# Optimization experiments

Measured on AMD Instinct MI355X. Metric: run time of the kernel, lower is better.

The kernel has to match this reference:

```python
import jax, jax.numpy as jnp
import numpy as np

K = 3       # kernel_size
STRIDE = 1
PAD = 1


def conv2d(x, w, b):
    y = jax.lax.conv_general_dilated(
        x, w, window_strides=(STRIDE, STRIDE), padding=[(PAD, PAD), (PAD, PAD)],
        dimension_numbers=('NCHW', 'OIHW', 'NCHW'))
    return y + b[None, :, None, None]


def setup_inputs() -> dict:
    key = jax.random.key(0)
    ks = jax.random.split(key, 4)
    B, Cin, Cout, H, W = 8, 64, 64, 64, 64
    kk = K * K
    x = jax.random.normal(ks[0], (B, Cin, H, W), jnp.float32)
    # offset / modulator convs (zero-init in the original; use small random weights
    # so offsets are nontrivial but realistic sub-pixel scale)
    w_off = jax.random.normal(ks[1], (2 * kk, Cin, K, K), jnp.float32) * 0.01
    b_off = jnp.zeros((2 * kk,), jnp.float32)
    w_mod = jax.random.normal(ks[2], (kk, Cin, K, K), jnp.float32) * 0.01
    b_mod = jnp.zeros((kk,), jnp.float32)
    # main deformable conv weight, Kaiming-ish scale
    w = jax.random.normal(ks[3], (Cout, Cin, K, K), jnp.float32) * (1.0 / np.sqrt(Cin * kk))
    b = jnp.zeros((Cout,), jnp.float32)
    return {"x": x, "w_off": w_off, "b_off": b_off,
            "w_mod": w_mod, "b_mod": b_mod, "w": w, "b": b}


def deform_conv2d(x, offset, mask, w, b):
    # torchvision deform_conv2d semantics, deformable_groups=1, groups=1.
    B, C, H, W = x.shape
    kk = K * K
    Ho = (H + 2 * PAD - K) // STRIDE + 1
    Wo = (W + 2 * PAD - K) // STRIDE + 1
    # offset channels are interleaved (dy, dx) pairs per kernel tap
    off = offset.reshape(B, kk, 2, Ho, Wo)
    kh, kw = jnp.meshgrid(jnp.arange(K), jnp.arange(K), indexing='ij')
    kh = kh.reshape(kk).astype(x.dtype)
    kw = kw.reshape(kk).astype(x.dtype)
    base_y = (jnp.arange(Ho) * STRIDE - PAD).astype(x.dtype)
    base_x = (jnp.arange(Wo) * STRIDE - PAD).astype(x.dtype)
    # sampling coordinates in input space: [B, kk, Ho, Wo]
    ys = base_y[None, None, :, None] + kh[None, :, None, None] + off[:, :, 0]
    xs = base_x[None, None, None, :] + kw[None, :, None, None] + off[:, :, 1]
    y0 = jnp.floor(ys)
    x0 = jnp.floor(xs)

    def gather(yi, xi):
        yc = jnp.clip(yi, 0, H - 1).astype(jnp.int32)
        xc = jnp.clip(xi, 0, W - 1).astype(jnp.int32)
        # per-batch fancy gather: [C, H, W] indexed by [kk, Ho, Wo] -> [C, kk, Ho, Wo]
        return jax.vmap(lambda img, yb, xb: img[:, yb, xb])(x, yc, xc)

    acc = jnp.zeros((B, C, kk, Ho, Wo), x.dtype)
    for dy, dx in ((0, 0), (0, 1), (1, 0), (1, 1)):
        yi = y0 + dy
        xi = x0 + dx
        wgt = (1.0 - jnp.abs(ys - yi)) * (1.0 - jnp.abs(xs - xi))
        # zero-padding semantics: corners outside the input contribute 0
        valid = (yi >= 0) & (yi <= H - 1) & (xi >= 0) & (xi <= W - 1)
        wgt = jnp.where(valid, wgt, 0.0)
        acc = acc + gather(yi, xi) * wgt[:, None]
    # modulate with sigmoid mask [B, kk, Ho, Wo], then contract with conv weight
    sampled = acc * mask[:, None]
    out = jnp.einsum('bcfij,ocf->boij', sampled, w.reshape(w.shape[0], C, kk))
    return out + b[None, :, None, None]


def reference(x, w_off, b_off, w_mod, b_mod, w, b):
    offset = conv2d(x, w_off, b_off)
    mask = jax.nn.sigmoid(conv2d(x, w_mod, b_mod))
    return deform_conv2d(x, offset, mask, w, b)
```

## Files before the change

### kernel.cpp

```cpp
#include <hip/hip_runtime.h>
#include <math.h>

#define HW    64
#define NPIX  32768

typedef __attribute__((ext_vector_type(8))) short bf16x8;
typedef __attribute__((ext_vector_type(8))) short short8v;
typedef __attribute__((ext_vector_type(4))) float f32x4;

static __device__ inline short f2bf(float f) {
    union { float f; unsigned u; } v; v.f = f;
    unsigned r = v.u + 0x7fff + ((v.u >> 16) & 1);
    return (short)(r >> 16);
}
static __device__ inline float bf2f(short s) {
    union { unsigned u; float f; } v; v.u = ((unsigned)(unsigned short)s) << 16;
    return v.f;
}

__global__ void k_prep(const float* __restrict__ w,
                       const float* __restrict__ w_off,
                       const float* __restrict__ w_mod,
                       short* __restrict__ wt2, short* __restrict__ wc2) {
    int t = blockIdx.x * 256 + threadIdx.x;
    if (t < 9 * 64 * 64) {
        int c = t & 63, o = (t >> 6) & 63, f = t >> 12;
        wt2[t] = f2bf(w[(o * 64 + c) * 9 + f]);
    }
    int u = t - 9 * 64 * 64;
    if (u >= 0 && u < 9 * 32 * 64) {
        int c = u & 63, ch = (u >> 6) & 31, f = u >> 11;
        float v = 0.f;
        if (ch < 18)      v = w_off[(ch * 64 + c) * 9 + f];
        else if (ch < 27) v = w_mod[((ch - 18) * 64 + c) * 9 + f];
        wc2[u] = f2bf(v);
    }
}

__global__ __launch_bounds__(256) void k_transpose(const float* __restrict__ x,
                                                   short* __restrict__ xt) {
    __shared__ float s[64 * 65];
    int tid = threadIdx.x;
    int by  = blockIdx.x;
    int b = by >> 6, y = by & 63;
    const float* xb = x + ((size_t)b * 64) * 4096 + y * 64;
    #pragma unroll
    for (int q = 0; q < 4; ++q) {
        int fi = q * 256 + tid;
        int c = fi >> 4, xq = (fi & 15) * 4;
        float4 v = *(const float4*)(xb + (size_t)c * 4096 + xq);
        s[c * 65 + xq + 0] = v.x; s[c * 65 + xq + 1] = v.y;
        s[c * 65 + xq + 2] = v.z; s[c * 65 + xq + 3] = v.w;
    }
    __syncthreads();
    short* dst = xt + ((size_t)(b * 64 + y)) * 4096;
    #pragma unroll
    for (int q = 0; q < 4; ++q) {
        int fi = q * 256 + tid;
        int xx = fi >> 4, c = (fi & 15) * 4;
        short4 v = make_short4(f2bf(s[(c + 0) * 65 + xx]), f2bf(s[(c + 1) * 65 + xx]),
                               f2bf(s[(c + 2) * 65 + xx]), f2bf(s[(c + 3) * 65 + xx]));
        *(short4*)(dst + xx * 64 + c) = v;
    }
}

__global__ __launch_bounds__(256) void k_convmeta(
        const short* __restrict__ xt, const short* __restrict__ wc2,
        const float* __restrict__ b_off, const float* __restrict__ b_mod,
        float4* __restrict__ metaW, int4* __restrict__ metaO) {
    __shared__ __align__(16) char smem[34816];
    float* s_out = (float*)(smem + 26112);

    int tid  = threadIdx.x;
    int lane = tid & 63;
    int wv   = __builtin_amdgcn_readfirstlane((int)(tid >> 6));
    int blk  = blockIdx.x;
    int b = blk >> 6, i = blk & 63;
    const short* xs = xt + (size_t)b * 262144;

    int arow = lane & 15, cg = lane >> 4, cgb = cg * 8;

    for (int u = tid; u < 1632; u += 256) {
        int cell = u >> 3, chunk = u & 7;
        int r = cell / 68, cc = cell - r * 68;
        int y = i - 1 + r, gx = cc - 2;
        short8v v = (short8v){0,0,0,0,0,0,0,0};
        if (((unsigned)y < 64u) & ((unsigned)gx < 64u))
            v = *(const short8v*)(xs + ((y << 6) + gx) * 64 + chunk * 8);
        *(short8v*)(smem + cell * 128 + ((chunk * 16) ^ ((cell & 7) << 4))) = v;
    }
    __syncthreads();

    {
        int nf = wv & 1, mg = wv >> 1;
        f32x4 accc[2];
        accc[0] = (f32x4){0.f,0.f,0.f,0.f};
        accc[1] = (f32x4){0.f,0.f,0.f,0.f};
        #pragma unroll
        for (int ky = 0; ky < 3; ++ky)
            #pragma unroll
            for (int kx = 0; kx < 3; ++kx) {
                int f = ky * 3 + kx;
                #pragma unroll
                for (int kk = 0; kk < 2; ++kk) {
                    bf16x8 bq = *(const bf16x8*)(wc2 + (f * 32 + nf * 16 + arow) * 64
                                                 + kk * 32 + cgb);
                    #pragma unroll
                    for (int mm = 0; mm < 2; ++mm) {
                        int cell = ky * 68 + mg * 32 + mm * 16 + arow + kx + 1;
                        const char* ap = smem + cell * 128
                                       + ((kk * 64 + cg * 16) ^ ((cell & 7) << 4));
                        accc[mm] = __builtin_amdgcn_mfma_f32_16x16x32_bf16(
                            *(const bf16x8*)ap, bq, accc[mm], 0, 0, 0);
                    }
                }
            }
        #pragma unroll
        for (int mm = 0; mm < 2; ++mm)
            #pragma unroll
            for (int r = 0; r < 4; ++r)
                s_out[(nf * 16 + arow) * 66 + mg * 32 + mm * 16 + cg * 4 + r] = accc[mm][r];
    }
    __syncthreads();

    int pixBase = blk * 64;
    for (int u = tid; u < 576; u += 256) {
        int f = u >> 6, p = u & 63;
        float dy = s_out[(2 * f)     * 66 + p] + b_off[2 * f];
        float dx = s_out[(2 * f + 1) * 66 + p] + b_off[2 * f + 1];
        float mv = s_out[(18 + f)    * 66 + p] + b_mod[f];
        float m  = 1.f / (1.f + expf(-mv));

        float ys  = (float)(i - 1 + f / 3) + dy;
        float xs2 = (float)(p - 1 + f % 3) + dx;
        float y0f = floorf(ys), x0f = floorf(xs2);
        int   y0  = (int)y0f,   x0  = (int)x0f;
        float fy = ys - y0f, fx = xs2 - x0f;

        bool vy0 = (unsigned)y0       < 64u, vy1 = (unsigned)(y0 + 1) < 64u;
        bool vx0 = (unsigned)x0       < 64u, vx1 = (unsigned)(x0 + 1) < 64u;
        float w00 = (vy0 & vx0) ? (1.f - fy) * (1.f - fx) * m : 0.f;
        float w01 = (vy0 & vx1) ? (1.f - fy) * fx         * m : 0.f;
        float w10 = (vy1 & vx0) ? fy         * (1.f - fx) * m : 0.f;
        float w11 = (vy1 & vx1) ? fy         * fx         * m : 0.f;

        int y0c = min(max(y0, 0), 63), y1c = min(max(y0 + 1, 0), 63);
        int x0c = min(max(x0, 0), 63), x1c = min(max(x0 + 1, 0), 63);

        metaW[f * NPIX + pixBase + p] = make_float4(w00, w01, w10, w11);
        metaO[f * NPIX + pixBase + p] = make_int4(((y0c << 6) + x0c) * 128,
                                                  ((y0c << 6) + x1c) * 128,
                                                  ((y1c << 6) + x0c) * 128,
                                                  ((y1c << 6) + x1c) * 128);
    }
}

__global__ __launch_bounds__(256) void k_sample(
        const short* __restrict__ xt,
        const float4* __restrict__ metaW, const int4* __restrict__ metaO,
        short* __restrict__ S) {
    int lane = threadIdx.x & 63;
    int wv   = __builtin_amdgcn_readfirstlane((int)(threadIdx.x >> 6));
    int wg   = blockIdx.x * 4 + wv;
    int t0   = wg * 36;
    #pragma unroll 6
    for (int it = 0; it < 36; ++it) {
        int t = t0 + it;
        float4 mW = metaW[t];
        int4   mO = metaO[t];
        int P = t & 32767;
        const char* xbb = (const char*)(xt + ((size_t)(P >> 12)) * 262144);
        short c0 = *(const short*)(xbb + mO.x + lane * 2);
        short c1 = *(const short*)(xbb + mO.y + lane * 2);
        short c2 = *(const short*)(xbb + mO.z + lane * 2);
        short c3 = *(const short*)(xbb + mO.w + lane * 2);
        float s = mW.x * bf2f(c0) + mW.y * bf2f(c1)
                + mW.z * bf2f(c2) + mW.w * bf2f(c3);
        S[(size_t)t * 64 + lane] = f2bf(s);
    }
}

__global__ __launch_bounds__(256, 4) void k_gemm(
        const short* __restrict__ S, const short* __restrict__ wt2,
        const float* __restrict__ bias, float* __restrict__ out) {
    __shared__ __align__(16) char smem[8448];
    float* s_fin = (float*)smem;

    int tid  = threadIdx.x;
    int lane = tid & 63;
    int wv   = __builtin_amdgcn_readfirstlane((int)(tid >> 6));
    int blk  = blockIdx.x;
    int b = blk >> 7, i = (blk >> 1) & 63, jb = (blk & 1) * 32;
    int P0 = blk * 32;

    int arow = lane & 15, cg = lane >> 4, cgb = cg * 8;

    bf16x8 bfrag[9][2];
    {
        int o = wv * 16 + arow;
        #pragma unroll
        for (int f = 0; f < 9; ++f)
            #pragma unroll
            for (int kk = 0; kk < 2; ++kk)
                bfrag[f][kk] = *(const bf16x8*)(wt2 + (f * 64 + o) * 64 + kk * 32 + cgb);
    }

    int spx = tid >> 3, schunk = tid & 7;
    int sdst = spx * 128 + ((schunk << 4) ^ ((spx & 7) << 4));
    #define SSRC(F) (S + ((size_t)(((F) << 15) + P0 + spx)) * 64 + schunk * 8)

    *(short8v*)(smem + sdst) = *(const short8v*)SSRC(0);
    __syncthreads();

    f32x4 acc[2];
    acc[0] = (f32x4){0.f,0.f,0.f,0.f};
    acc[1] = (f32x4){0.f,0.f,0.f,0.f};

    for (int f = 0; f < 9; ++f) {
        int curb = (f & 1) * 4096;
        short8v ldv;
        if (f < 8) ldv = *(const short8v*)SSRC(f + 1);
        #pragma unroll
        for (int kk = 0; kk < 2; ++kk)
            #pragma unroll
            for (int mf = 0; mf < 2; ++mf) {
                int px = mf * 16 + arow;
                const char* ap = smem + curb + px * 128
                               + ((kk * 64 + cg * 16) ^ ((px & 7) << 4));
                acc[mf] = __builtin_amdgcn_mfma_f32_16x16x32_bf16(
                    *(const bf16x8*)ap, bfrag[f][kk], acc[mf], 0, 0, 0);
            }
        if (f < 8) *(short8v*)(smem + (curb ^ 4096) + sdst) = ldv;
        __syncthreads();
    }
    #undef SSRC

    {
        int o = wv * 16 + arow;
        #pragma unroll
        for (int mf = 0; mf < 2; ++mf)
            #pragma unroll
            for (int r = 0; r < 4; ++r)
                s_fin[o * 33 + mf * 16 + cg * 4 + r] = acc[mf][r];
    }
    __syncthreads();
    {
        int o = tid >> 2, q = tid & 3;
        float bv = bias[o];
        float* op = out + ((size_t)(b * 64 + o)) * 4096 + i * 64 + jb + q * 8;
        float4 v0, v1;
        v0.x = s_fin[o * 33 + q * 8 + 0] + bv;
        v0.y = s_fin[o * 33 + q * 8 + 1] + bv;
        v0.z = s_fin[o * 33 + q * 8 + 2] + bv;
        v0.w = s_fin[o * 33 + q * 8 + 3] + bv;
        v1.x = s_fin[o * 33 + q * 8 + 4] + bv;
        v1.y = s_fin[o * 33 + q * 8 + 5] + bv;
        v1.z = s_fin[o * 33 + q * 8 + 6] + bv;
        v1.w = s_fin[o * 33 + q * 8 + 7] + bv;
        *(float4*)op       = v0;
        *(float4*)(op + 4) = v1;
    }
}

extern "C" void kernel_launch(void* const* d_in, const int* in_sizes, int n_in,
                              void* d_out, int out_size, void* d_ws, size_t ws_size,
                              hipStream_t stream) {
    const float* x     = (const float*)d_in[0];
    const float* w_off = (const float*)d_in[1];
    const float* b_off = (const float*)d_in[2];
    const float* w_mod = (const float*)d_in[3];
    const float* b_mod = (const float*)d_in[4];
    const float* w     = (const float*)d_in[5];
    const float* bias  = (const float*)d_in[6];
    float* out = (float*)d_out;

    char* ws = (char*)d_ws;
    short*  xt    = (short*)(ws);
    short*  wt2   = (short*)(ws + 4194304);
    short*  wc2   = (short*)(ws + 4268032);
    float4* metaW = (float4*)(ws + 4304896);
    int4*   metaO = (int4*)(ws + 9023488);
    short*  S     = (short*)(ws + 13742080);

    hipLaunchKernelGGL(k_prep,      dim3(216),  dim3(256), 0, stream, w, w_off, w_mod, wt2, wc2);
    hipLaunchKernelGGL(k_transpose, dim3(512),  dim3(256), 0, stream, x, xt);
    hipLaunchKernelGGL(k_convmeta,  dim3(512),  dim3(256), 0, stream,
                       xt, wc2, b_off, b_mod, metaW, metaO);
    hipLaunchKernelGGL(k_sample,    dim3(2048), dim3(256), 0, stream,
                       xt, metaW, metaO, S);
    hipLaunchKernelGGL(k_gemm,      dim3(1024), dim3(256), 0, stream,
                       S, wt2, bias, out);
}
```

Baseline: 61.53 us.

## Fuse bilinear sampling into GEMM kernel and merge prep with transpose

The bilinear sampling stage is moved into the MFMA GEMM kernel. Each block samples its 32 pixels for all 9 taps straight into a swizzled shared-memory tile, so the intermediate S buffer is no longer written to and read back from global memory. The weight prep and input transpose kernels are merged into one launch, and the main weights are pre-laid out in fragment order so each lane loads its fragment contiguously. The cost is 36KB of shared memory per block and the loss of the previous double-buffered pipelining of sample loads against MFMA, which may reduce occupancy and latency hiding.

```diff
diff --git a/kernel.cpp b/kernel.cpp
--- a/kernel.cpp
+++ b/kernel.cpp
@@ -18,49 +18,54 @@
     return v.f;
 }
 
-__global__ void k_prep(const float* __restrict__ w,
-                       const float* __restrict__ w_off,
-                       const float* __restrict__ w_mod,
-                       short* __restrict__ wt2, short* __restrict__ wc2) {
-    int t = blockIdx.x * 256 + threadIdx.x;
-    if (t < 9 * 64 * 64) {
-        int c = t & 63, o = (t >> 6) & 63, f = t >> 12;
-        wt2[t] = f2bf(w[(o * 64 + c) * 9 + f]);
-    }
-    int u = t - 9 * 64 * 64;
-    if (u >= 0 && u < 9 * 32 * 64) {
-        int c = u & 63, ch = (u >> 6) & 31, f = u >> 11;
-        float v = 0.f;
-        if (ch < 18)      v = w_off[(ch * 64 + c) * 9 + f];
-        else if (ch < 27) v = w_mod[((ch - 18) * 64 + c) * 9 + f];
-        wc2[u] = f2bf(v);
-    }
-}
-
-__global__ __launch_bounds__(256) void k_transpose(const float* __restrict__ x,
-                                                   short* __restrict__ xt) {
-    __shared__ float s[64 * 65];
+__global__ __launch_bounds__(256) void k_misc(
+        const float* __restrict__ x, short* __restrict__ xt,
+        const float* __restrict__ w, const float* __restrict__ w_off,
+        const float* __restrict__ w_mod,
+        short* __restrict__ wt3, short* __restrict__ wc2) {
     int tid = threadIdx.x;
-    int by  = blockIdx.x;
-    int b = by >> 6, y = by & 63;
-    const float* xb = x + ((size_t)b * 64) * 4096 + y * 64;
-    #pragma unroll
-    for (int q = 0; q < 4; ++q) {
-        int fi = q * 256 + tid;
-        int c = fi >> 4, xq = (fi & 15) * 4;
-        float4 v = *(const float4*)(xb + (size_t)c * 4096 + xq);
-        s[c * 65 + xq + 0] = v.x; s[c * 65 + xq + 1] = v.y;
-        s[c * 65 + xq + 2] = v.z; s[c * 65 + xq + 3] = v.w;
-    }
-    __syncthreads();
-    short* dst = xt + ((size_t)(b * 64 + y)) * 4096;
-    #pragma unroll
-    for (int q = 0; q < 4; ++q) {
-        int fi = q * 256 + tid;
-        int xx = fi >> 4, c = (fi & 15) * 4;
-        short4 v = make_short4(f2bf(s[(c + 0) * 65 + xx]), f2bf(s[(c + 1) * 65 + xx]),
-                               f2bf(s[(c + 2) * 65 + xx]), f2bf(s[(c + 3) * 65 + xx]));
-        *(short4*)(dst + xx * 64 + c) = v;
+    if (blockIdx.x < 512) {
+        __shared__ float s[64 * 65];
+        int by = blockIdx.x;
+        int b = by >> 6, y = by & 63;
+        const float* xb = x + ((size_t)b * 64) * 4096 + y * 64;
+        #pragma unroll
+        for (int q = 0; q < 4; ++q) {
+            int fi = q * 256 + tid;
+            int c = fi >> 4, xq = (fi & 15) * 4;
+            float4 v = *(const float4*)(xb + (size_t)c * 4096 + xq);
+            s[c * 65 + xq + 0] = v.x; s[c * 65 + xq + 1] = v.y;
+            s[c * 65 + xq + 2] = v.z; s[c * 65 + xq + 3] = v.w;
+        }
+        __syncthreads();
+        short* dst = xt + ((size_t)(b * 64 + y)) * 4096;
+        #pragma unroll
+        for (int q = 0; q < 4; ++q) {
+            int fi = q * 256 + tid;
+            int xx = fi >> 4, c = (fi & 15) * 4;
+            short4 v = make_short4(f2bf(s[(c + 0) * 65 + xx]), f2bf(s[(c + 1) * 65 + xx]),
+                                   f2bf(s[(c + 2) * 65 + xx]), f2bf(s[(c + 3) * 65 + xx]));
+            *(short4*)(dst + xx * 64 + c) = v;
+        }
+    } else {
+        int t = (blockIdx.x - 512) * 256 + tid;
+        if (t < 36864) {
+            int wv = t / 9216, r = t - wv * 9216;
+            int f  = r >> 10;
+            int r2 = r & 1023;
+            int kk = r2 >> 9, lane = (r2 >> 3) & 63, j = r2 & 7;
+            int o = wv * 16 + (lane & 15);
+            int c = kk * 32 + (lane >> 4) * 8 + j;
+            wt3[t] = f2bf(w[(o * 64 + c) * 9 + f]);
+        }
+        int u = t - 36864;
+        if (u >= 0 && u < 9 * 32 * 64) {
+            int c = u & 63, ch = (u >> 6) & 31, f = u >> 11;
+            float v = 0.f;
+            if (ch < 18)      v = w_off[(ch * 64 + c) * 9 + f];
+            else if (ch < 27) v = w_mod[((ch - 18) * 64 + c) * 9 + f];
+            wc2[u] = f2bf(v);
+        }
     }
 }
 
@@ -155,35 +160,12 @@
     }
 }
 
-__global__ __launch_bounds__(256) void k_sample(
+__global__ __launch_bounds__(256, 4) void k_deform(
         const short* __restrict__ xt,
         const float4* __restrict__ metaW, const int4* __restrict__ metaO,
-        short* __restrict__ S) {
-    int lane = threadIdx.x & 63;
-    int wv   = __builtin_amdgcn_readfirstlane((int)(threadIdx.x >> 6));
-    int wg   = blockIdx.x * 4 + wv;
-    int t0   = wg * 36;
-    #pragma unroll 6
-    for (int it = 0; it < 36; ++it) {
-        int t = t0 + it;
-        float4 mW = metaW[t];
-        int4   mO = metaO[t];
-        int P = t & 32767;
-        const char* xbb = (const char*)(xt + ((size_t)(P >> 12)) * 262144);
-        short c0 = *(const short*)(xbb + mO.x + lane * 2);
-        short c1 = *(const short*)(xbb + mO.y + lane * 2);
-        short c2 = *(const short*)(xbb + mO.z + lane * 2);
-        short c3 = *(const short*)(xbb + mO.w + lane * 2);
-        float s = mW.x * bf2f(c0) + mW.y * bf2f(c1)
-                + mW.z * bf2f(c2) + mW.w * bf2f(c3);
-        S[(size_t)t * 64 + lane] = f2bf(s);
-    }
-}
-
-__global__ __launch_bounds__(256, 4) void k_gemm(
-        const short* __restrict__ S, const short* __restrict__ wt2,
-        const float* __restrict__ bias, float* __restrict__ out) {
-    __shared__ __align__(16) char smem[8448];
+        const short* __restrict__ wt3, const float* __restrict__ bias,
+        float* __restrict__ out) {
+    __shared__ __align__(16) char smem[36864];
     float* s_fin = (float*)smem;
 
     int tid  = threadIdx.x;
@@ -192,48 +174,53 @@
     int blk  = blockIdx.x;
     int b = blk >> 7, i = (blk >> 1) & 63, jb = (blk & 1) * 32;
     int P0 = blk * 32;
-
-    int arow = lane & 15, cg = lane >> 4, cgb = cg * 8;
+    int arow = lane & 15, cg = lane >> 4;
 
     bf16x8 bfrag[9][2];
-    {
-        int o = wv * 16 + arow;
-        #pragma unroll
-        for (int f = 0; f < 9; ++f)
-            #pragma unroll
-            for (int kk = 0; kk < 2; ++kk)
-                bfrag[f][kk] = *(const bf16x8*)(wt2 + (f * 64 + o) * 64 + kk * 32 + cgb);
-    }
-
-    int spx = tid >> 3, schunk = tid & 7;
-    int sdst = spx * 128 + ((schunk << 4) ^ ((spx & 7) << 4));
-    #define SSRC(F) (S + ((size_t)(((F) << 15) + P0 + spx)) * 64 + schunk * 8)
-
-    *(short8v*)(smem + sdst) = *(const short8v*)SSRC(0);
+    #pragma unroll
+    for (int f = 0; f < 9; ++f)
+        #pragma unroll
+        for (int kk = 0; kk < 2; ++kk)
+            bfrag[f][kk] = *(const bf16x8*)(wt3 + ((wv * 18 + f * 2 + kk) * 64 + lane) * 8);
+
+    #pragma unroll
+    for (int pp = 0; pp < 8; ++pp) {
+        int px = wv * 8 + pp;
+        int P  = P0 + px;
+        const char* xbb = (const char*)(xt + ((size_t)(P >> 12)) * 262144);
+        int rowbase = px * 1152;
+        int swz = (px & 7) << 4;
+        #pragma unroll
+        for (int f = 0; f < 9; ++f) {
+            float4 mW = metaW[f * NPIX + P];
+            int4   mO = metaO[f * NPIX + P];
+            short c0 = *(const short*)(xbb + mO.x + lane * 2);
+            short c1 = *(const short*)(xbb + mO.y + lane * 2);
+            short c2 = *(const short*)(xbb + mO.z + lane * 2);
+            short c3 = *(const short*)(xbb + mO.w + lane * 2);
+            float s = mW.x * bf2f(c0) + mW.y * bf2f(c1)
+                    + mW.z * bf2f(c2) + mW.w * bf2f(c3);
+            *(short*)(smem + rowbase + f * 128 + ((lane * 2) ^ swz)) = f2bf(s);
+        }
+    }
     __syncthreads();
 
     f32x4 acc[2];
     acc[0] = (f32x4){0.f,0.f,0.f,0.f};
     acc[1] = (f32x4){0.f,0.f,0.f,0.f};
-
-    for (int f = 0; f < 9; ++f) {
-        int curb = (f & 1) * 4096;
-        short8v ldv;
-        if (f < 8) ldv = *(const short8v*)SSRC(f + 1);
+    #pragma unroll
+    for (int f = 0; f < 9; ++f)
         #pragma unroll
         for (int kk = 0; kk < 2; ++kk)
             #pragma unroll
             for (int mf = 0; mf < 2; ++mf) {
                 int px = mf * 16 + arow;
-                const char* ap = smem + curb + px * 128
+                const char* ap = smem + px * 1152 + f * 128
                                + ((kk * 64 + cg * 16) ^ ((px & 7) << 4));
                 acc[mf] = __builtin_amdgcn_mfma_f32_16x16x32_bf16(
                     *(const bf16x8*)ap, bfrag[f][kk], acc[mf], 0, 0, 0);
             }
-        if (f < 8) *(short8v*)(smem + (curb ^ 4096) + sdst) = ldv;
-        __syncthreads();
-    }
-    #undef SSRC
+    __syncthreads();
 
     {
         int o = wv * 16 + arow;
@@ -276,18 +263,15 @@
 
     char* ws = (char*)d_ws;
     short*  xt    = (short*)(ws);
-    short*  wt2   = (short*)(ws + 4194304);
+    short*  wt3   = (short*)(ws + 4194304);
     short*  wc2   = (short*)(ws + 4268032);
     float4* metaW = (float4*)(ws + 4304896);
     int4*   metaO = (int4*)(ws + 9023488);
-    short*  S     = (short*)(ws + 13742080);
-
-    hipLaunchKernelGGL(k_prep,      dim3(216),  dim3(256), 0, stream, w, w_off, w_mod, wt2, wc2);
-    hipLaunchKernelGGL(k_transpose, dim3(512),  dim3(256), 0, stream, x, xt);
+
+    hipLaunchKernelGGL(k_misc,      dim3(728),  dim3(256), 0, stream,
+                       x, xt, w, w_off, w_mod, wt3, wc2);
     hipLaunchKernelGGL(k_convmeta,  dim3(512),  dim3(256), 0, stream,
                        xt, wc2, b_off, b_mod, metaW, metaO);
-    hipLaunchKernelGGL(k_sample,    dim3(2048), dim3(256), 0, stream,
-                       xt, metaW, metaO, S);
-    hipLaunchKernelGGL(k_gemm,      dim3(1024), dim3(256), 0, stream,
-                       S, wt2, bias, out);
-}
+    hipLaunchKernelGGL(k_deform,    dim3(1024), dim3(256), 0, stream,
+                       xt, metaW, metaO, wt3, bias, out);
+}
```

After: 79.43 us. 29.1% more time.
